# Kernel tuning notes

Hardware: AMD Instinct MI355X
Metric: run time of the kernel (lower is better)

The kernel has to match this reference:

```python
import jax, jax.numpy as jnp
import numpy as np

N_THRESHOLDS = 10


def setup_inputs() -> dict:
    key = jax.random.key(0)
    k1, k2, k3 = jax.random.split(key, 3)
    shape = (32, 1024, 1024)
    prediction = jax.random.normal(k1, shape, dtype=jnp.float32)
    mask = jax.random.randint(k2, shape, 0, 2, dtype=jnp.int32)
    target = jax.random.randint(k3, shape, 0, 2, dtype=jnp.int32)
    return {"prediction": prediction, "mask": mask, "target": target}


def reference(prediction, mask, target):
    # thresholds = linspace(0,1,n+2)[1:-1], same as the torch module
    thresholds = jnp.linspace(0.0, 1.0, N_THRESHOLDS + 2, dtype=jnp.float32)[1:-1]

    s = jax.nn.sigmoid(prediction).ravel()            # [N]
    m = mask.ravel().astype(bool)                     # [N] valid mask
    t = target.ravel().astype(bool)                   # [N]
    mt = m & t                                        # masked positives

    # Broadcast compare against all thresholds at once (single fused pass,
    # no per-threshold host sync like the original loop).
    pos = s[None, :] > thresholds[:, None]            # [T, N] bool

    tp = jnp.sum(pos & mt[None, :], axis=1)           # [T] int32
    p = jnp.sum(pos & m[None, :], axis=1)             # predicted-positive count

    total_m = jnp.sum(m)                              # total valid elements
    total_t = jnp.sum(mt)                             # total true positives in mask

    fp = p - tp
    fn = total_t - tp
    tn = total_m - p - fn

    # classes layout matches torch module: rows = [tp, fp, tn, fn]
    return jnp.stack([tp, fp, tn, fn], axis=0).astype(jnp.float32)
```

## Files before the change

### kernel.cpp

```cpp
#include <hip/hip_runtime.h>


#define NTHR 10
#define NCNT 22
#define WS_STRIDE 16

__device__ __forceinline__ unsigned wave_reduce_add(unsigned v) {
#pragma unroll
    for (int off = 32; off > 0; off >>= 1)
        v += __shfl_down(v, off, 64);
    return v;
}

__global__ __launch_bounds__(64) void zero_ws_kernel(unsigned* __restrict__ ws) {
    int i = threadIdx.x;
    if (i < NCNT) ws[i * WS_STRIDE] = 0u;
}

__global__ __launch_bounds__(256) void count_kernel(
        const float4* __restrict__ pred4,
        const int4*  __restrict__ mask4,
        const int4*  __restrict__ targ4,
        const float* __restrict__ pred,
        const int*   __restrict__ mask,
        const int*   __restrict__ targ,
        unsigned* __restrict__ ws, int nvec, int n) {
    const float L[NTHR] = {-2.3025851f, -1.5040774f, -0.98082925f, -0.55961579f,
                           -0.18232156f, 0.18232156f,  0.55961579f,  0.98082925f,
                            1.5040774f,  2.3025851f};
    unsigned accTP[NTHR] = {}, accP[NTHR] = {};
    unsigned accM = 0u, accMT = 0u;

    const int idx    = blockIdx.x * blockDim.x + threadIdx.x;
    const int stride = gridDim.x * blockDim.x;

    for (int i = idx; i < nvec; i += stride) {
        float4 p = pred4[i];
        int4   m = mask4[i];
        int4   t = targ4[i];
        float    pv[4] = {p.x, p.y, p.z, p.w};
        unsigned mv[4] = {(unsigned)m.x, (unsigned)m.y, (unsigned)m.z, (unsigned)m.w};
        unsigned tv[4] = {(unsigned)t.x, (unsigned)t.y, (unsigned)t.z, (unsigned)t.w};
#pragma unroll
        for (int c = 0; c < 4; ++c) {
            unsigned mm = mv[c];
            unsigned mt = mm & tv[c];
            accM  += mm;
            accMT += mt;
#pragma unroll
            for (int j = 0; j < NTHR; ++j) {
                bool pos = pv[c] > L[j];
                accP[j]  += pos ? mm : 0u;
                accTP[j] += pos ? mt : 0u;
            }
        }
    }
    int rem = n & 3;
    if (idx < rem) {
        int i = nvec * 4 + idx;
        float    pv = pred[i];
        unsigned mm = (unsigned)mask[i];
        unsigned mt = mm & (unsigned)targ[i];
        accM += mm; accMT += mt;
#pragma unroll
        for (int j = 0; j < NTHR; ++j) {
            bool pos = pv > L[j];
            accP[j]  += pos ? mm : 0u;
            accTP[j] += pos ? mt : 0u;
        }
    }

    unsigned vals[NCNT];
#pragma unroll
    for (int j = 0; j < NTHR; ++j) { vals[j] = accTP[j]; vals[NTHR + j] = accP[j]; }
    vals[20] = accM;
    vals[21] = accMT;
#pragma unroll
    for (int c = 0; c < NCNT; ++c) vals[c] = wave_reduce_add(vals[c]);

    __shared__ unsigned partial[4][NCNT];
    const int wave = threadIdx.x >> 6;
    const int lane = threadIdx.x & 63;
    if (lane == 0) {
#pragma unroll
        for (int c = 0; c < NCNT; ++c) partial[wave][c] = vals[c];
    }
    __syncthreads();
    if (threadIdx.x < NCNT) {
        unsigned s = partial[0][threadIdx.x] + partial[1][threadIdx.x] +
                     partial[2][threadIdx.x] + partial[3][threadIdx.x];
        atomicAdd(&ws[threadIdx.x * WS_STRIDE], s);
    }
}

__global__ __launch_bounds__(64) void finalize_kernel(const unsigned* __restrict__ ws,
                                                      float* __restrict__ out) {
    int j = threadIdx.x;
    if (j < NTHR) {
        unsigned tp = ws[j * WS_STRIDE];
        unsigned p  = ws[(NTHR + j) * WS_STRIDE];
        unsigned tm = ws[20 * WS_STRIDE];
        unsigned tt = ws[21 * WS_STRIDE];
        unsigned fp = p - tp;
        unsigned fn = tt - tp;
        unsigned tn = tm - p - fn;
        out[j]            = (float)tp;
        out[NTHR + j]     = (float)fp;
        out[2 * NTHR + j] = (float)tn;
        out[3 * NTHR + j] = (float)fn;
    }
}

extern "C" void kernel_launch(void* const* d_in, const int* in_sizes, int n_in,
                              void* d_out, int out_size, void* d_ws, size_t ws_size,
                              hipStream_t stream) {
    const float* pred = (const float*)d_in[0];
    const int*   mask = (const int*)d_in[1];
    const int*   targ = (const int*)d_in[2];
    unsigned*    ws   = (unsigned*)d_ws;
    float*       out  = (float*)d_out;

    const int n    = in_sizes[0];
    const int nvec = n / 4;

    zero_ws_kernel<<<1, 64, 0, stream>>>(ws);

    const int blocks = 2048;
    count_kernel<<<blocks, 256, 0, stream>>>(
        (const float4*)pred, (const int4*)mask, (const int4*)targ,
        pred, mask, targ, ws, nvec, n);

    finalize_kernel<<<1, 64, 0, stream>>>(ws, out);
}
```

Baseline: 364.0 us.

## Bucket predictions into packed 5-bit histogram counters instead of per-threshold accumulators

```diff
diff --git a/kernel.cpp b/kernel.cpp
--- a/kernel.cpp
+++ b/kernel.cpp
@@ -2,6 +2,7 @@
 
 
 #define NTHR 10
+#define NBKT 11
 #define NCNT 22
 #define WS_STRIDE 16
 
@@ -17,6 +18,30 @@
     if (i < NCNT) ws[i * WS_STRIDE] = 0u;
 }
 
+__device__ __forceinline__ void proc_elem(float pv, unsigned mm, unsigned tt,
+                                          const float* L,
+                                          unsigned long long& hP,
+                                          unsigned long long& hT) {
+    unsigned mt = mm & tt;
+    unsigned b = 0u;
+#pragma unroll
+    for (int j = 0; j < NTHR; ++j) b += (pv > L[j]) ? 1u : 0u;
+    unsigned sh = (b << 2) + b;
+    hP += (unsigned long long)mm << sh;
+    hT += (unsigned long long)mt << sh;
+}
+
+__device__ __forceinline__ void flush_hist(unsigned long long& hP,
+                                           unsigned long long& hT,
+                                           unsigned* cP, unsigned* cT) {
+#pragma unroll
+    for (int b = 0; b < NBKT; ++b) {
+        cP[b] += (unsigned)(hP >> (5 * b)) & 31u;
+        cT[b] += (unsigned)(hT >> (5 * b)) & 31u;
+    }
+    hP = 0ull; hT = 0ull;
+}
+
 __global__ __launch_bounds__(256) void count_kernel(
         const float4* __restrict__ pred4,
         const int4*  __restrict__ mask4,
@@ -24,57 +49,50 @@
         const float* __restrict__ pred,
         const int*   __restrict__ mask,
         const int*   __restrict__ targ,
-        unsigned* __restrict__ ws, int nvec, int n) {
+        unsigned* __restrict__ ws, int half, int n) {
     const float L[NTHR] = {-2.3025851f, -1.5040774f, -0.98082925f, -0.55961579f,
                            -0.18232156f, 0.18232156f,  0.55961579f,  0.98082925f,
                             1.5040774f,  2.3025851f};
-    unsigned accTP[NTHR] = {}, accP[NTHR] = {};
-    unsigned accM = 0u, accMT = 0u;
+    unsigned cP[NBKT] = {}, cT[NBKT] = {};
+    unsigned long long hP = 0ull, hT = 0ull;
 
     const int idx    = blockIdx.x * blockDim.x + threadIdx.x;
     const int stride = gridDim.x * blockDim.x;
 
-    for (int i = idx; i < nvec; i += stride) {
-        float4 p = pred4[i];
-        int4   m = mask4[i];
-        int4   t = targ4[i];
-        float    pv[4] = {p.x, p.y, p.z, p.w};
-        unsigned mv[4] = {(unsigned)m.x, (unsigned)m.y, (unsigned)m.z, (unsigned)m.w};
-        unsigned tv[4] = {(unsigned)t.x, (unsigned)t.y, (unsigned)t.z, (unsigned)t.w};
-#pragma unroll
-        for (int c = 0; c < 4; ++c) {
-            unsigned mm = mv[c];
-            unsigned mt = mm & tv[c];
-            accM  += mm;
-            accMT += mt;
-#pragma unroll
-            for (int j = 0; j < NTHR; ++j) {
-                bool pos = pv[c] > L[j];
-                accP[j]  += pos ? mm : 0u;
-                accTP[j] += pos ? mt : 0u;
-            }
-        }
+    int fcnt = 0;
+    for (int i = idx; i < half; i += stride) {
+        float4 p0 = pred4[i];
+        float4 p1 = pred4[i + half];
+        int4   m0 = mask4[i];
+        int4   m1 = mask4[i + half];
+        int4   t0 = targ4[i];
+        int4   t1 = targ4[i + half];
+
+        proc_elem(p0.x, (unsigned)m0.x, (unsigned)t0.x, L, hP, hT);
+        proc_elem(p0.y, (unsigned)m0.y, (unsigned)t0.y, L, hP, hT);
+        proc_elem(p0.z, (unsigned)m0.z, (unsigned)t0.z, L, hP, hT);
+        proc_elem(p0.w, (unsigned)m0.w, (unsigned)t0.w, L, hP, hT);
+        proc_elem(p1.x, (unsigned)m1.x, (unsigned)t1.x, L, hP, hT);
+        proc_elem(p1.y, (unsigned)m1.y, (unsigned)t1.y, L, hP, hT);
+        proc_elem(p1.z, (unsigned)m1.z, (unsigned)t1.z, L, hP, hT);
+        proc_elem(p1.w, (unsigned)m1.w, (unsigned)t1.w, L, hP, hT);
+
+        if (++fcnt == 3) { flush_hist(hP, hT, cP, cT); fcnt = 0; }
     }
-    int rem = n & 3;
-    if (idx < rem) {
-        int i = nvec * 4 + idx;
-        float    pv = pred[i];
-        unsigned mm = (unsigned)mask[i];
-        unsigned mt = mm & (unsigned)targ[i];
-        accM += mm; accMT += mt;
-#pragma unroll
-        for (int j = 0; j < NTHR; ++j) {
-            bool pos = pv > L[j];
-            accP[j]  += pos ? mm : 0u;
-            accTP[j] += pos ? mt : 0u;
+    flush_hist(hP, hT, cP, cT);
+
+    {
+        int tail_base = half * 8;
+        int i = tail_base + idx;
+        if (i < n) {
+            proc_elem(pred[i], (unsigned)mask[i], (unsigned)targ[i], L, hP, hT);
+            flush_hist(hP, hT, cP, cT);
         }
     }
 
     unsigned vals[NCNT];
 #pragma unroll
-    for (int j = 0; j < NTHR; ++j) { vals[j] = accTP[j]; vals[NTHR + j] = accP[j]; }
-    vals[20] = accM;
-    vals[21] = accMT;
+    for (int b = 0; b < NBKT; ++b) { vals[b] = cP[b]; vals[NBKT + b] = cT[b]; }
 #pragma unroll
     for (int c = 0; c < NCNT; ++c) vals[c] = wave_reduce_add(vals[c]);
 
@@ -97,13 +115,17 @@
                                                       float* __restrict__ out) {
     int j = threadIdx.x;
     if (j < NTHR) {
-        unsigned tp = ws[j * WS_STRIDE];
-        unsigned p  = ws[(NTHR + j) * WS_STRIDE];
-        unsigned tm = ws[20 * WS_STRIDE];
-        unsigned tt = ws[21 * WS_STRIDE];
+        unsigned totM = 0u, totT = 0u, p = 0u, tp = 0u;
+#pragma unroll
+        for (int b = 0; b < NBKT; ++b) {
+            unsigned vP = ws[b * WS_STRIDE];
+            unsigned vT = ws[(NBKT + b) * WS_STRIDE];
+            totM += vP; totT += vT;
+            if (b > j) { p += vP; tp += vT; }
+        }
         unsigned fp = p - tp;
-        unsigned fn = tt - tp;
-        unsigned tn = tm - p - fn;
+        unsigned fn = totT - tp;
+        unsigned tn = totM - p - fn;
         out[j]            = (float)tp;
         out[NTHR + j]     = (float)fp;
         out[2 * NTHR + j] = (float)tn;
@@ -122,13 +144,14 @@
 
     const int n    = in_sizes[0];
     const int nvec = n / 4;
+    const int half = nvec / 2;
 
     zero_ws_kernel<<<1, 64, 0, stream>>>(ws);
 
     const int blocks = 2048;
     count_kernel<<<blocks, 256, 0, stream>>>(
         (const float4*)pred, (const int4*)mask, (const int4*)targ,
-        pred, mask, targ, ws, nvec, n);
+        pred, mask, targ, ws, half, n);
 
     finalize_kernel<<<1, 64, 0, stream>>>(ws, out);
 }
```

After: 362.9 us. No clear change (-0.3%).
